# Optimization experiments

Measured on AMD Instinct MI355X. Metric: run time of the kernel, lower is better.

Reference implementation:

```python
import jax, jax.numpy as jnp
import numpy as np

DIM = 768
HEADS = 12
HEAD_DIM = DIM // HEADS
WS = 14  # window size
MLP = 3072
EPS = 1e-6
SCALE = HEAD_DIM ** -0.5
B, H, W = 4, 64, 64


def setup_inputs() -> dict:
    key = jax.random.key(0)
    ks = jax.random.split(key, 8)
    s = 0.02
    f32 = jnp.float32
    return {
        "hidden_states": jax.random.normal(ks[0], (B, DIM, H, W), f32),
        "ln1_w": jnp.ones((DIM,), f32),
        "ln1_b": jnp.zeros((DIM,), f32),
        "qkv_w": jax.random.normal(ks[1], (DIM, 3 * DIM), f32) * s,
        "qkv_b": jnp.zeros((3 * DIM,), f32),
        "proj_w": jax.random.normal(ks[2], (DIM, DIM), f32) * s,
        "proj_b": jnp.zeros((DIM,), f32),
        "rel_pos_h": jax.random.normal(ks[3], (2 * WS - 1, HEAD_DIM), f32) * s,
        "rel_pos_w": jax.random.normal(ks[4], (2 * WS - 1, HEAD_DIM), f32) * s,
        "ln2_w": jnp.ones((DIM,), f32),
        "ln2_b": jnp.zeros((DIM,), f32),
        "fc1_w": jax.random.normal(ks[5], (DIM, MLP), f32) * s,
        "fc1_b": jnp.zeros((MLP,), f32),
        "fc2_w": jax.random.normal(ks[6], (MLP, DIM), f32) * s,
        "fc2_b": jnp.zeros((DIM,), f32),
    }


def _layer_norm(x, w, b):
    mu = jnp.mean(x, axis=-1, keepdims=True)
    var = jnp.mean(jnp.square(x - mu), axis=-1, keepdims=True)
    return (x - mu) * jax.lax.rsqrt(var + EPS) * w + b


def _get_rel_pos(size, rel_pos):
    # q_size == k_size == WS, rel_pos already has 2*WS-1 rows -> pure gather
    coords = jnp.arange(size)[:, None] - jnp.arange(size)[None, :] + (size - 1)
    return rel_pos[coords]  # (size, size, head_dim)


def _attention(x, qkv_w, qkv_b, proj_w, proj_b, rel_pos_h, rel_pos_w):
    nb, h, w, c = x.shape  # windows batch, WS, WS, DIM
    n = h * w
    qkv = x.reshape(nb, n, c) @ qkv_w + qkv_b  # (nb, n, 3*DIM)
    qkv = qkv.reshape(nb, n, 3, HEADS, HEAD_DIM).transpose(2, 0, 3, 1, 4)
    qkv = qkv.reshape(3, nb * HEADS, n, HEAD_DIM)
    q, k, v = qkv[0], qkv[1], qkv[2]
    attn = jnp.einsum('bqc,bkc->bqk', q * SCALE, k)  # (nb*HEADS, n, n)
    # decomposed relative position bias
    Rh = _get_rel_pos(h, rel_pos_h)  # (h, h, hd)
    Rw = _get_rel_pos(w, rel_pos_w)  # (w, w, hd)
    rq = q.reshape(-1, h, w, HEAD_DIM)
    rel_h = jnp.einsum('bhwc,hkc->bhwk', rq, Rh)
    rel_w = jnp.einsum('bhwc,wkc->bhwk', rq, Rw)
    attn = (attn.reshape(-1, h, w, h, w)
            + rel_h[:, :, :, :, None]
            + rel_w[:, :, :, None, :]).reshape(-1, n, n)
    attn = jax.nn.softmax(attn, axis=-1)
    out = attn @ v  # (nb*HEADS, n, hd)
    out = out.reshape(nb, HEADS, h, w, HEAD_DIM).transpose(0, 2, 3, 1, 4)
    out = out.reshape(nb, h, w, c)
    return out @ proj_w + proj_b


def reference(hidden_states, ln1_w, ln1_b, qkv_w, qkv_b, proj_w, proj_b,
              rel_pos_h, rel_pos_w, ln2_w, ln2_b, fc1_w, fc1_b, fc2_w, fc2_b):
    x = hidden_states.transpose(0, 2, 3, 1)  # NCHW -> NHWC
    b, h, w, c = x.shape
    shortcut = x
    x = _layer_norm(x, ln1_w, ln1_b)
    # window partition with padding
    ph = (WS - h % WS) % WS
    pw = (WS - w % WS) % WS
    x = jnp.pad(x, ((0, 0), (0, ph), (0, pw), (0, 0)))
    hp, wp = h + ph, w + pw
    x = x.reshape(b, hp // WS, WS, wp // WS, WS, c).transpose(0, 1, 3, 2, 4, 5)
    windows = x.reshape(-1, WS, WS, c)
    windows = _attention(windows, qkv_w, qkv_b, proj_w, proj_b, rel_pos_h, rel_pos_w)
    # window unpartition + crop
    x = windows.reshape(b, hp // WS, wp // WS, WS, WS, c).transpose(0, 1, 3, 2, 4, 5)
    x = x.reshape(b, hp, wp, c)[:, :h, :w, :]
    x = shortcut + x
    y = _layer_norm(x, ln2_w, ln2_b)
    y = jax.nn.gelu(y @ fc1_w + fc1_b, approximate=False) @ fc2_w + fc2_b
    x = x + y
    return x.transpose(0, 3, 1, 2)  # back to NCHW
```

## Files before the change

kernel.cpp:

```cpp
#include <hip/hip_runtime.h>
#include <cstdint>
#include <cstddef>

#define NIMG   4
#define GRIDSZ 64
#define CH     768
#define NHEAD  12
#define WSZ    14
#define NWINS  100
#define NTOK   196
#define MWIN   19600
#define MREAL  16384
#define MLPC   3072
#define QKSCALE 0.125f

#define KSTR 72
#define VSTR 216
#define PSTR 40

typedef unsigned short u16;
typedef __attribute__((ext_vector_type(8))) short bf16x8;
typedef __attribute__((ext_vector_type(4))) float f32x4;

__device__ __forceinline__ float b2f(u16 u) {
  uint32_t x = (uint32_t)u << 16; float f; __builtin_memcpy(&f, &x, 4); return f;
}
__device__ __forceinline__ u16 f2b(float f) {
  uint32_t x; __builtin_memcpy(&x, &f, 4);
  x += 0x7fffu + ((x >> 16) & 1u);
  return (u16)(x >> 16);
}

__device__ __forceinline__ float fast_gelu(float x) {
  float z  = x * 0.70710678118654752440f;
  float az = fabsf(z);
  float t  = 1.0f / (1.0f + 0.3275911f * az);
  float poly = ((((1.061405429f * t - 1.453152027f) * t + 1.421413741f) * t
                 - 0.284496736f) * t + 0.254829592f) * t;
  float e  = __expf(-az * az);
  float erfv = copysignf(1.0f - poly * e, z);
  return 0.5f * x * (1.0f + erfv);
}

__device__ __forceinline__ void gl_lds16(const u16* g, u16* l) {
  __builtin_amdgcn_global_load_lds(
      (const __attribute__((address_space(1))) unsigned int*)g,
      (__attribute__((address_space(3))) unsigned int*)l, 16, 0, 0);
}

__global__ __launch_bounds__(256) void k_nchw2nhwc(const float* __restrict__ in,
                                                   float* __restrict__ out) {
  __shared__ float tile[32][33];
  int b  = blockIdx.z;
  int g0 = blockIdx.x * 32;
  int c0 = blockIdx.y * 32;
  int tx = threadIdx.x, ty = threadIdx.y;
  const float* ip = in + (size_t)b * CH * 4096;
  float* op = out + (size_t)b * 4096 * CH;
#pragma unroll
  for (int k = 0; k < 32; k += 8)
    tile[ty + k][tx] = ip[(size_t)(c0 + ty + k) * 4096 + g0 + tx];
  __syncthreads();
#pragma unroll
  for (int k = 0; k < 32; k += 8)
    op[(size_t)(g0 + ty + k) * CH + c0 + tx] = tile[tx][ty + k];
}

__global__ __launch_bounds__(256) void k_nhwc2nchw(const float* __restrict__ in,
                                                   float* __restrict__ out) {
  __shared__ float tile[32][33];
  int b  = blockIdx.z;
  int g0 = blockIdx.x * 32;
  int c0 = blockIdx.y * 32;
  int tx = threadIdx.x, ty = threadIdx.y;
  const float* ip = in + (size_t)b * 4096 * CH;
  float* op = out + (size_t)b * CH * 4096;
#pragma unroll
  for (int k = 0; k < 32; k += 8)
    tile[ty + k][tx] = ip[(size_t)(g0 + ty + k) * CH + c0 + tx];
  __syncthreads();
#pragma unroll
  for (int k = 0; k < 32; k += 8)
    op[(size_t)(c0 + ty + k) * 4096 + g0 + tx] = tile[tx][ty + k];
}

__global__ __launch_bounds__(256) void k_wt(const float* __restrict__ in,
                                            u16* __restrict__ out,
                                            int K, int N) {
  __shared__ float t[32][33];
  int n0 = blockIdx.x * 32, k0 = blockIdx.y * 32;
  int tx = threadIdx.x, ty = threadIdx.y;
#pragma unroll
  for (int k = 0; k < 32; k += 8)
    t[ty + k][tx] = in[(size_t)(k0 + ty + k) * N + n0 + tx];
  __syncthreads();
#pragma unroll
  for (int k = 0; k < 32; k += 8)
    out[(size_t)(n0 + ty + k) * K + k0 + tx] = f2b(t[tx][ty + k]);
}

__device__ __forceinline__ float block_sum(float s, float* red) {
  __syncthreads();
#pragma unroll
  for (int off = 32; off > 0; off >>= 1) s += __shfl_down(s, off, 64);
  int wid = threadIdx.x >> 6, lane = threadIdx.x & 63;
  if (lane == 0) red[wid] = s;
  __syncthreads();
  return red[0] + red[1] + red[2] + red[3];
}

__global__ __launch_bounds__(256) void k_ln(const float* __restrict__ x,
                                            const float* __restrict__ wt,
                                            const float* __restrict__ bs,
                                            u16* __restrict__ y,
                                            int window_mode) {
  __shared__ float red[4];
  int row = blockIdx.x, tid = threadIdx.x;
  const float* xp = x + (size_t)row * CH;
  float v0 = xp[tid], v1 = xp[tid + 256], v2 = xp[tid + 512];
  float mu = block_sum(v0 + v1 + v2, red) * (1.0f / 768.0f);
  float d0 = v0 - mu, d1 = v1 - mu, d2 = v2 - mu;
  float var = block_sum(d0 * d0 + d1 * d1 + d2 * d2, red) * (1.0f / 768.0f);
  float rs = rsqrtf(var + 1e-6f);
  int orow = row;
  if (window_mode) {
    int b = row >> 12, hw = row & 4095;
    int h = hw >> 6, wc = hw & 63;
    orow = (b * 25 + (h / WSZ) * 5 + (wc / WSZ)) * NTOK + (h % WSZ) * WSZ + (wc % WSZ);
  }
  u16* yp = y + (size_t)orow * CH;
  yp[tid]       = f2b(d0 * rs * wt[tid]       + bs[tid]);
  yp[tid + 256] = f2b(d1 * rs * wt[tid + 256] + bs[tid + 256]);
  yp[tid + 512] = f2b(d2 * rs * wt[tid + 512] + bs[tid + 512]);
}

__global__ __launch_bounds__(256, 2) void k_gemm_mfma(const u16* __restrict__ A,
                                                      const u16* __restrict__ BT,
                                                      const float* __restrict__ bias,
                                                      void* __restrict__ Cv,
                                                      u16* __restrict__ Vt,
                                                      int M, int N, int K,
                                                      int act, int mode, int row0) {
  __shared__ u16 As[3][256 * 32];
  __shared__ u16 Bs[3][128 * 32];
  int tid  = threadIdx.x;
  int lane = tid & 63, wave = tid >> 6;

  int gx   = gridDim.x;
  int nwg  = gx * gridDim.y;
  int orig = blockIdx.y * gx + blockIdx.x;
  int q = nwg >> 3, r = nwg & 7;
  int xcd = orig & 7, idx = orig >> 3;
  int wgid = (xcd < r ? xcd * (q + 1) : r * (q + 1) + (xcd - r) * q) + idx;
  int bn = wgid % gx, bm = wgid / gx;

  int wm = (wave & 1) * 128, wn = (wave >> 1) * 64;
  int l15 = lane & 15, quad = lane >> 4;
  int xq = (quad ^ ((l15 >> 1) & 3)) * 8;

  f32x4 acc[8][4];
#pragma unroll
  for (int i = 0; i < 8; i++)
#pragma unroll
    for (int j = 0; j < 4; j++) acc[i][j] = (f32x4){0.f, 0.f, 0.f, 0.f};

  const u16* Atile = A + (size_t)bm * 256 * K;
  const u16* Btile = BT + (size_t)bn * 128 * K;

  const int nk = K >> 5;

#define STAGE_SLAB(slot, slab)                                               \
  do {                                                                       \
    int kk_ = (slab) << 5;                                                   \
    _Pragma("unroll")                                                        \
    for (int i = 0; i < 4; ++i) {                                            \
      int c_ = i * 256 + wave * 64 + lane;                                   \
      int row_ = c_ >> 2, gs_ = (c_ & 3) ^ ((c_ >> 3) & 3);                  \
      gl_lds16(Atile + (size_t)row_ * K + kk_ + gs_ * 8,                     \
               &As[(slot)][(i * 256 + wave * 64) * 8]);                      \
    }                                                                        \
    _Pragma("unroll")                                                        \
    for (int i = 0; i < 2; ++i) {                                            \
      int c_ = i * 256 + wave * 64 + lane;                                   \
      int row_ = c_ >> 2, gs_ = (c_ & 3) ^ ((c_ >> 3) & 3);                  \
      gl_lds16(Btile + (size_t)row_ * K + kk_ + gs_ * 8,                     \
               &Bs[(slot)][(i * 256 + wave * 64) * 8]);                      \
    }                                                                        \
  } while (0)

#define COMPUTE_SLAB(slot)                                                   \
  do {                                                                       \
    bf16x8 af[8], bfv[4];                                                    \
    _Pragma("unroll")                                                        \
    for (int mi = 0; mi < 8; mi++)                                           \
      af[mi] = *(const bf16x8*)&As[(slot)][(size_t)(wm + mi * 16 + l15) * 32 \
                                           + xq];                            \
    _Pragma("unroll")                                                        \
    for (int ni = 0; ni < 4; ni++)                                           \
      bfv[ni] = *(const bf16x8*)&Bs[(slot)][(size_t)(wn + ni * 16 + l15) * 32\
                                            + xq];                           \
    _Pragma("unroll")                                                        \
    for (int mi = 0; mi < 8; mi++)                                           \
      _Pragma("unroll")                                                      \
      for (int ni = 0; ni < 4; ni++)                                         \
        acc[mi][ni] = __builtin_amdgcn_mfma_f32_16x16x32_bf16(               \
            bfv[ni], af[mi], acc[mi][ni], 0, 0, 0);                          \
  } while (0)

  STAGE_SLAB(0, 0);
  STAGE_SLAB(1, 1);

  int t = 0;
  for (; t < nk - 1; ++t) {
    asm volatile("s_waitcnt vmcnt(6)" ::: "memory");
    __builtin_amdgcn_s_barrier();
    __builtin_amdgcn_sched_barrier(0);
    if (t + 2 < nk) STAGE_SLAB((t + 2) % 3, t + 2);
    COMPUTE_SLAB(t % 3);
  }
  asm volatile("s_waitcnt vmcnt(0)" ::: "memory");
  __builtin_amdgcn_s_barrier();
  __builtin_amdgcn_sched_barrier(0);
  COMPUTE_SLAB(t % 3);

#undef STAGE_SLAB
#undef COMPUTE_SLAB

#pragma unroll
  for (int mi = 0; mi < 8; mi++) {
    int row = bm * 256 + wm + mi * 16 + l15;
    if (row >= M) continue;
    size_t gbase = 0;
    bool valid = true;
    int wloc = 0, tok = 0;
    if (mode == 2) {
      int rowa = row + row0;
      int widx = rowa / NTOK, tt = rowa % NTOK;
      int b = widx / 25, wq = widx % 25;
      int h = (wq / 5) * WSZ + tt / WSZ;
      int w = (wq % 5) * WSZ + tt % WSZ;
      valid = (h < GRIDSZ) && (w < GRIDSZ);
      gbase = valid ? ((size_t)((b * GRIDSZ + h) * GRIDSZ + w)) * CH : 0;
    }
    if (mode == 3) { wloc = row / NTOK; tok = row - wloc * NTOK; }
#pragma unroll
    for (int ni = 0; ni < 4; ni++) {
      int colb = bn * 128 + wn + ni * 16 + quad * 4;
      float4 b4 = *(const float4*)&bias[colb];
      float v[4] = {acc[mi][ni][0] + b4.x, acc[mi][ni][1] + b4.y,
                    acc[mi][ni][2] + b4.z, acc[mi][ni][3] + b4.w};
      if (act == 1) {
#pragma unroll
        for (int r2 = 0; r2 < 4; r2++) v[r2] = fast_gelu(v[r2]);
      }
      if (mode == 0) {
        ushort4 st = make_ushort4(f2b(v[0]), f2b(v[1]), f2b(v[2]), f2b(v[3]));
        *(ushort4*)((u16*)Cv + (size_t)row * N + colb) = st;
      } else if (mode == 1) {
        float4* p = (float4*)((float*)Cv + (size_t)row * N + colb);
        float4 o = *p;
        o.x += v[0]; o.y += v[1]; o.z += v[2]; o.w += v[3];
        *p = o;
      } else if (mode == 2) {
        if (valid) {
          float4* p = (float4*)((float*)Cv + gbase + colb);
          float4 o = *p;
          o.x += v[0]; o.y += v[1]; o.z += v[2]; o.w += v[3];
          *p = o;
        }
      } else {
        if (colb < 1536) {
          ushort4 st = make_ushort4(f2b(v[0]), f2b(v[1]), f2b(v[2]), f2b(v[3]));
          *(ushort4*)((u16*)Cv + (size_t)row * N + colb) = st;
        } else {
          int vv = colb - 1536, hd = vv >> 6, d = vv & 63;
          u16* vp = Vt + ((size_t)(wloc * NHEAD + hd) * 64 + d) * VSTR + tok;
#pragma unroll
          for (int r2 = 0; r2 < 4; r2++) vp[(size_t)r2 * VSTR] = f2b(v[r2]);
        }
      }
    }
  }
}

__global__ __launch_bounds__(256) void k_relbias(const u16* __restrict__ qkv,
                                                 const float* __restrict__ rel_h,
                                                 const float* __restrict__ rel_w,
                                                 u16* __restrict__ rhg,
                                                 u16* __restrict__ rwg,
                                                 int nrows) {
  int idx = blockIdx.x * 256 + threadIdx.x;
  if (idx >= nrows * NHEAD) return;
  int head = idx % NHEAD, row = idx / NHEAD;
  int wloc = row / NTOK, tok = row - wloc * NTOK;
  const u16* qp = qkv + (size_t)row * (3 * CH) + head * 64;
  float q[64];
#pragma unroll
  for (int d = 0; d < 64; d += 4) {
    ushort4 u4 = *(const ushort4*)(qp + d);
    q[d] = b2f(u4.x); q[d + 1] = b2f(u4.y); q[d + 2] = b2f(u4.z); q[d + 3] = b2f(u4.w);
  }
  int hq = tok / WSZ, wq = tok % WSZ;
  size_t obase = ((size_t)(wloc * NHEAD + head) * NTOK + tok) * 16;
  for (int kk = 0; kk < WSZ; kk++) {
    const float* rh = rel_h + (size_t)(hq - kk + WSZ - 1) * 64;
    const float* rw = rel_w + (size_t)(wq - kk + WSZ - 1) * 64;
    float sh = 0.0f, sw = 0.0f;
#pragma unroll
    for (int d = 0; d < 64; d++) { sh += q[d] * rh[d]; sw += q[d] * rw[d]; }
    rhg[obase + kk] = f2b(sh);
    rwg[obase + kk] = f2b(sw);
  }
}

__global__ __launch_bounds__(256) void k_attn_mfma(const u16* __restrict__ qkv,
                                                   const u16* __restrict__ Vt,
                                                   const u16* __restrict__ rhg,
                                                   const u16* __restrict__ rwg,
                                                   u16* __restrict__ out,
                                                   int win0) {
  __shared__ u16 Ks[NTOK * KSTR];
  __shared__ u16 Vs[64 * VSTR];
  __shared__ u16 Ps[4][16 * PSTR];
  int head = blockIdx.x, wloc = blockIdx.y;
  int tid = threadIdx.x, lane = tid & 63, wave = tid >> 6;
  int l15 = lane & 15, quad = lane >> 4;
  const u16* qbase = qkv + (size_t)wloc * NTOK * (3 * CH) + head * 64;

  for (int c = tid; c < NTOK * 8; c += 256) {
    int tok = c >> 3, part = c & 7;
    uint4 v = *(const uint4*)(qbase + (size_t)tok * (3 * CH) + CH + part * 8);
    *(uint4*)&Ks[tok * KSTR + part * 8] = v;
  }
  const u16* vb = Vt + (size_t)(wloc * NHEAD + head) * 64 * VSTR;
#pragma unroll
  for (int it = 0; it < 7; ++it) {
    int c = it * 256 + tid;
    if (c < 64 * VSTR / 8) gl_lds16(vb + (size_t)c * 8, Vs + ((size_t)it * 256 + wave * 64) * 8);
  }
  __syncthreads();

  const u16* rhp = rhg + ((size_t)(wloc * NHEAD + head) * NTOK) * 16;
  const u16* rwp = rwg + ((size_t)(wloc * NHEAD + head) * NTOK) * 16;
  int winabs = win0 + wloc;

  for (int t16 = wave; t16 < 13; t16 += 4) {
    int qtok = t16 * 16 + l15; if (qtok > NTOK - 1) qtok = NTOK - 1;
    bf16x8 aq0 = *(const bf16x8*)(qbase + (size_t)qtok * (3 * CH) + quad * 8);
    bf16x8 aq1 = *(const bf16x8*)(qbase + (size_t)qtok * (3 * CH) + 32 + quad * 8);

    f32x4 s[13];
#pragma unroll
    for (int ct = 0; ct < 13; ct++) s[ct] = (f32x4){0.f, 0.f, 0.f, 0.f};
#pragma unroll
    for (int ct = 0; ct < 13; ct++) {
      int ktok = ct * 16 + l15; if (ktok > NTOK - 1) ktok = NTOK - 1;
      bf16x8 bk0 = *(const bf16x8*)&Ks[ktok * KSTR + quad * 8];
      bf16x8 bk1 = *(const bf16x8*)&Ks[ktok * KSTR + 32 + quad * 8];
      s[ct] = __builtin_amdgcn_mfma_f32_16x16x32_bf16(aq0, bk0, s[ct], 0, 0, 0);
      s[ct] = __builtin_amdgcn_mfma_f32_16x16x32_bf16(aq1, bk1, s[ct], 0, 0, 0);
    }

    f32x4 o[4];
#pragma unroll
    for (int ni = 0; ni < 4; ni++) o[ni] = (f32x4){0.f, 0.f, 0.f, 0.f};
    float lsum[4] = {0.f, 0.f, 0.f, 0.f};
    int row0t = t16 * 16 + quad * 4;

#pragma unroll
    for (int cc = 0; cc < 7; ++cc) {
#pragma unroll
      for (int half = 0; half < 2; ++half) {
        int ct = cc * 2 + half;
        if (ct < 13) {
          int col = ct * 16 + l15;
          int jh = col / WSZ, jw = col - jh * WSZ;
          bool colok = col < NTOK;
#pragma unroll
          for (int r = 0; r < 4; r++) {
            int rowt = row0t + r; int rowc = rowt > NTOK - 1 ? NTOK - 1 : rowt;
            float bias = b2f(rhp[rowc * 16 + jh]) + b2f(rwp[rowc * 16 + jw]);
            float sv = s[ct][r] * QKSCALE + bias;
            float p = colok ? __expf(sv) : 0.f;
            lsum[r] += p;
            Ps[wave][(quad * 4 + r) * PSTR + half * 16 + l15] = f2b(p);
          }
        } else {
#pragma unroll
          for (int r = 0; r < 4; r++)
            Ps[wave][(quad * 4 + r) * PSTR + half * 16 + l15] = 0;
        }
      }
      bf16x8 pa = *(const bf16x8*)&Ps[wave][l15 * PSTR + quad * 8];
#pragma unroll
      for (int ni = 0; ni < 4; ni++) {
        bf16x8 bv = *(const bf16x8*)&Vs[(ni * 16 + l15) * VSTR + cc * 32 + quad * 8];
        o[ni] = __builtin_amdgcn_mfma_f32_16x16x32_bf16(pa, bv, o[ni], 0, 0, 0);
      }
    }

#pragma unroll
    for (int r = 0; r < 4; r++) {
#pragma unroll
      for (int m = 1; m < 16; m <<= 1) lsum[r] += __shfl_xor(lsum[r], m, 64);
    }

#pragma unroll
    for (int r = 0; r < 4; r++) {
      int rowt = row0t + r;
      if (rowt < NTOK) {
        float inv = 1.0f / lsum[r];
        u16* op = out + ((size_t)winabs * NTOK + rowt) * CH + head * 64;
#pragma unroll
        for (int ni = 0; ni < 4; ni++) op[ni * 16 + l15] = f2b(o[ni][r] * inv);
      }
    }
  }
}

extern "C" void kernel_launch(void* const* d_in, const int* in_sizes, int n_in,
                              void* d_out, int out_size, void* d_ws, size_t ws_size,
                              hipStream_t stream) {
  const float* hidden = (const float*)d_in[0];
  const float* ln1_w  = (const float*)d_in[1];
  const float* ln1_b  = (const float*)d_in[2];
  const float* qkv_w  = (const float*)d_in[3];
  const float* qkv_b  = (const float*)d_in[4];
  const float* proj_w = (const float*)d_in[5];
  const float* proj_b = (const float*)d_in[6];
  const float* rel_h  = (const float*)d_in[7];
  const float* rel_w  = (const float*)d_in[8];
  const float* ln2_w  = (const float*)d_in[9];
  const float* ln2_b  = (const float*)d_in[10];
  const float* fc1_w  = (const float*)d_in[11];
  const float* fc1_b  = (const float*)d_in[12];
  const float* fc2_w  = (const float*)d_in[13];
  const float* fc2_b  = (const float*)d_in[14];
  float* out = (float*)d_out;

  char* ws = (char*)d_ws;
  float* x_nhwc = (float*)ws;
  u16*   R1     = (u16*)(ws + 50331648);
  u16*   qkvT   = (u16*)(ws + 80437248);
  u16*   projT  = qkvT + (size_t)2304 * 768;
  u16*   fc1T   = projT + (size_t)768 * 768;
  u16*   fc2T   = fc1T + (size_t)3072 * 768;
  u16*   R2     = fc2T + (size_t)768 * 3072;
  size_t used   = (size_t)80437248 + 14155776;
  size_t r2e    = ws_size > used ? (ws_size - used) >> 1 : 0;

  const size_t PW_QKV = (size_t)NTOK * 3 * CH;
  const size_t PW_VT  = (size_t)NHEAD * 64 * VSTR;
  const size_t PW_RB  = (size_t)NHEAD * NTOK * 16;
  const size_t perwin = PW_QKV + PW_VT + 2 * PW_RB;
  size_t wc_s = r2e / perwin;
  int Wc = wc_s >= NWINS ? NWINS : (int)wc_s;
  if (Wc < 1) Wc = 1;
  size_t rc_s = (r2e / MLPC / 256) * 256;
  int Rc = rc_s >= MREAL ? MREAL : (int)rc_s;
  if (Rc < 256) Rc = 256;

  u16* Vt  = R2 + (size_t)Wc * PW_QKV;
  u16* rhg = Vt + (size_t)Wc * PW_VT;
  u16* rwg = rhg + (size_t)Wc * PW_RB;

  k_wt<<<dim3(72, 24), dim3(32, 8), 0, stream>>>(qkv_w, qkvT, CH, 3 * CH);
  k_wt<<<dim3(24, 24), dim3(32, 8), 0, stream>>>(proj_w, projT, CH, CH);
  k_wt<<<dim3(96, 24), dim3(32, 8), 0, stream>>>(fc1_w, fc1T, CH, MLPC);
  k_wt<<<dim3(24, 96), dim3(32, 8), 0, stream>>>(fc2_w, fc2T, MLPC, CH);

  hipMemsetAsync(R1, 0, (size_t)MWIN * CH * sizeof(u16), stream);

  k_nchw2nhwc<<<dim3(128, 24, NIMG), dim3(32, 8), 0, stream>>>(hidden, x_nhwc);
  k_ln<<<MREAL, 256, 0, stream>>>(x_nhwc, ln1_w, ln1_b, R1, 1);
  for (int w0 = 0; w0 < NWINS; w0 += Wc) {
    int wc = NWINS - w0 < Wc ? NWINS - w0 : Wc;
    int Mc = wc * NTOK;
    k_gemm_mfma<<<dim3(18, (Mc + 255) / 256), 256, 0, stream>>>(
        R1 + (size_t)w0 * NTOK * CH, qkvT, qkv_b, R2, Vt,
        Mc, 3 * CH, CH, 0, 3, 0);
    k_relbias<<<(Mc * NHEAD + 255) / 256, 256, 0, stream>>>(
        R2, rel_h, rel_w, rhg, rwg, Mc);
    k_attn_mfma<<<dim3(NHEAD, wc), 256, 0, stream>>>(
        R2, Vt, rhg, rwg, R1, w0);
  }
  k_gemm_mfma<<<dim3(6, (MWIN + 255) / 256), 256, 0, stream>>>(
      R1, projT, proj_b, x_nhwc, nullptr, MWIN, CH, CH, 0, 2, 0);
  k_ln<<<MREAL, 256, 0, stream>>>(x_nhwc, ln2_w, ln2_b, R1, 0);
  for (int r0 = 0; r0 < MREAL; r0 += Rc) {
    int rc = MREAL - r0 < Rc ? MREAL - r0 : Rc;
    k_gemm_mfma<<<dim3(24, (rc + 255) / 256), 256, 0, stream>>>(
        R1 + (size_t)r0 * CH, fc1T, fc1_b, R2, nullptr, rc, MLPC, CH, 1, 0, 0);
    k_gemm_mfma<<<dim3(6, (rc + 255) / 256), 256, 0, stream>>>(
        R2, fc2T, fc2_b, x_nhwc + (size_t)r0 * CH, nullptr, rc, CH, MLPC, 0, 1, 0);
  }
  k_nhwc2nchw<<<dim3(128, 24, NIMG), dim3(32, 8), 0, stream>>>(x_nhwc, out);
}
```

Baseline: 765.9 us.

## Template GEMM on M-tile size and use 128-row tiles for narrow-N GEMMs

Turns the MFMA GEMM into a template over the M-tile height and occupancy hint. The N=768 GEMMs (proj and fc2) now use 128-row tiles with three blocks per CU, giving more workgroups to fill the GPU. The k-loop is also unrolled by three so the LDS slot indices are compile-time constants, and the per-slab global addresses are precomputed pointers that are bumped each step. The trade-off is lower reuse per tile in the smaller variant, and the unrolled loop assumes the K-slab count fits the three-slot pattern.

```diff
diff --git a/kernel.cpp b/kernel.cpp
--- a/kernel.cpp
+++ b/kernel.cpp
@@ -134,14 +134,18 @@
   yp[tid + 512] = f2b(d2 * rs * wt[tid + 512] + bs[tid + 512]);
 }
 
-__global__ __launch_bounds__(256, 2) void k_gemm_mfma(const u16* __restrict__ A,
+template <int BMT, int MINB>
+__global__ __launch_bounds__(256, MINB) void k_gemm_t(const u16* __restrict__ A,
                                                       const u16* __restrict__ BT,
                                                       const float* __restrict__ bias,
                                                       void* __restrict__ Cv,
                                                       u16* __restrict__ Vt,
                                                       int M, int N, int K,
                                                       int act, int mode, int row0) {
-  __shared__ u16 As[3][256 * 32];
+  constexpr int MI = BMT / 32;
+  constexpr int LA = BMT / 64;
+  constexpr int L  = LA + 2;
+  __shared__ u16 As[3][BMT * 32];
   __shared__ u16 Bs[3][128 * 32];
   int tid  = threadIdx.x;
   int lane = tid & 63, wave = tid >> 6;
@@ -154,81 +158,95 @@
   int wgid = (xcd < r ? xcd * (q + 1) : r * (q + 1) + (xcd - r) * q) + idx;
   int bn = wgid % gx, bm = wgid / gx;
 
-  int wm = (wave & 1) * 128, wn = (wave >> 1) * 64;
+  int wm = (wave & 1) * (BMT / 2), wn = (wave >> 1) * 64;
   int l15 = lane & 15, quad = lane >> 4;
   int xq = (quad ^ ((l15 >> 1) & 3)) * 8;
 
-  f32x4 acc[8][4];
-#pragma unroll
-  for (int i = 0; i < 8; i++)
+  f32x4 acc[MI][4];
+#pragma unroll
+  for (int i = 0; i < MI; i++)
 #pragma unroll
     for (int j = 0; j < 4; j++) acc[i][j] = (f32x4){0.f, 0.f, 0.f, 0.f};
 
-  const u16* Atile = A + (size_t)bm * 256 * K;
+  const u16* Atile = A + (size_t)bm * BMT * K;
   const u16* Btile = BT + (size_t)bn * 128 * K;
 
+  const u16* ga[LA];
+  const u16* gb[2];
+#pragma unroll
+  for (int i = 0; i < LA; ++i) {
+    int c_ = i * 256 + wave * 64 + lane;
+    int row_ = c_ >> 2, gs_ = (c_ & 3) ^ ((c_ >> 3) & 3);
+    ga[i] = Atile + (size_t)row_ * K + gs_ * 8;
+  }
+#pragma unroll
+  for (int i = 0; i < 2; ++i) {
+    int c_ = i * 256 + wave * 64 + lane;
+    int row_ = c_ >> 2, gs_ = (c_ & 3) ^ ((c_ >> 3) & 3);
+    gb[i] = Btile + (size_t)row_ * K + gs_ * 8;
+  }
+
   const int nk = K >> 5;
 
-#define STAGE_SLAB(slot, slab)                                               \
+#define STAGE(slot)                                                          \
   do {                                                                       \
-    int kk_ = (slab) << 5;                                                   \
     _Pragma("unroll")                                                        \
-    for (int i = 0; i < 4; ++i) {                                            \
-      int c_ = i * 256 + wave * 64 + lane;                                   \
-      int row_ = c_ >> 2, gs_ = (c_ & 3) ^ ((c_ >> 3) & 3);                  \
-      gl_lds16(Atile + (size_t)row_ * K + kk_ + gs_ * 8,                     \
-               &As[(slot)][(i * 256 + wave * 64) * 8]);                      \
+    for (int i = 0; i < LA; ++i) {                                           \
+      gl_lds16(ga[i], &As[(slot)][(i * 256 + wave * 64) * 8]);               \
+      ga[i] += 32;                                                           \
     }                                                                        \
     _Pragma("unroll")                                                        \
     for (int i = 0; i < 2; ++i) {                                            \
-      int c_ = i * 256 + wave * 64 + lane;                                   \
-      int row_ = c_ >> 2, gs_ = (c_ & 3) ^ ((c_ >> 3) & 3);                  \
-      gl_lds16(Btile + (size_t)row_ * K + kk_ + gs_ * 8,                     \
-               &Bs[(slot)][(i * 256 + wave * 64) * 8]);                      \
+      gl_lds16(gb[i], &Bs[(slot)][(i * 256 + wave * 64) * 8]);               \
+      gb[i] += 32;                                                           \
     }                                                                        \
   } while (0)
 
-#define COMPUTE_SLAB(slot)                                                   \
+#define COMPUTE(slot)                                                        \
   do {                                                                       \
-    bf16x8 af[8], bfv[4];                                                    \
+    bf16x8 af[MI], bfv[4];                                                   \
     _Pragma("unroll")                                                        \
-    for (int mi = 0; mi < 8; mi++)                                           \
-      af[mi] = *(const bf16x8*)&As[(slot)][(size_t)(wm + mi * 16 + l15) * 32 \
-                                           + xq];                            \
+    for (int mi = 0; mi < MI; mi++)                                          \
+      af[mi] = *(const bf16x8*)&As[(slot)][(wm + mi * 16 + l15) * 32 + xq];  \
     _Pragma("unroll")                                                        \
     for (int ni = 0; ni < 4; ni++)                                           \
-      bfv[ni] = *(const bf16x8*)&Bs[(slot)][(size_t)(wn + ni * 16 + l15) * 32\
-                                            + xq];                           \
+      bfv[ni] = *(const bf16x8*)&Bs[(slot)][(wn + ni * 16 + l15) * 32 + xq]; \
     _Pragma("unroll")                                                        \
-    for (int mi = 0; mi < 8; mi++)                                           \
+    for (int mi = 0; mi < MI; mi++)                                          \
       _Pragma("unroll")                                                      \
       for (int ni = 0; ni < 4; ni++)                                         \
         acc[mi][ni] = __builtin_amdgcn_mfma_f32_16x16x32_bf16(               \
             bfv[ni], af[mi], acc[mi][ni], 0, 0, 0);                          \
   } while (0)
 
-  STAGE_SLAB(0, 0);
-  STAGE_SLAB(1, 1);
-
-  int t = 0;
-  for (; t < nk - 1; ++t) {
-    asm volatile("s_waitcnt vmcnt(6)" ::: "memory");
-    __builtin_amdgcn_s_barrier();
-    __builtin_amdgcn_sched_barrier(0);
-    if (t + 2 < nk) STAGE_SLAB((t + 2) % 3, t + 2);
-    COMPUTE_SLAB(t % 3);
-  }
+#define WAITL                                                                \
+  do {                                                                       \
+    if constexpr (L == 6) asm volatile("s_waitcnt vmcnt(6)" ::: "memory");   \
+    else                  asm volatile("s_waitcnt vmcnt(4)" ::: "memory");   \
+    __builtin_amdgcn_s_barrier();                                            \
+  } while (0)
+
+  STAGE(0);
+  STAGE(1);
+
+  for (int g = 0; g < nk - 3; g += 3) {
+    WAITL; STAGE(2); COMPUTE(0);
+    WAITL; STAGE(0); COMPUTE(1);
+    WAITL; STAGE(1); COMPUTE(2);
+  }
+  WAITL; STAGE(2); COMPUTE(0);
+  WAITL;           COMPUTE(1);
   asm volatile("s_waitcnt vmcnt(0)" ::: "memory");
   __builtin_amdgcn_s_barrier();
-  __builtin_amdgcn_sched_barrier(0);
-  COMPUTE_SLAB(t % 3);
-
-#undef STAGE_SLAB
-#undef COMPUTE_SLAB
-
-#pragma unroll
-  for (int mi = 0; mi < 8; mi++) {
-    int row = bm * 256 + wm + mi * 16 + l15;
+  COMPUTE(2);
+
+#undef STAGE
+#undef COMPUTE
+#undef WAITL
+
+#pragma unroll
+  for (int mi = 0; mi < MI; mi++) {
+    int row = bm * BMT + wm + mi * 16 + l15;
     if (row >= M) continue;
     size_t gbase = 0;
     bool valid = true;
@@ -476,7 +494,7 @@
   for (int w0 = 0; w0 < NWINS; w0 += Wc) {
     int wc = NWINS - w0 < Wc ? NWINS - w0 : Wc;
     int Mc = wc * NTOK;
-    k_gemm_mfma<<<dim3(18, (Mc + 255) / 256), 256, 0, stream>>>(
+    k_gemm_t<256, 2><<<dim3(18, (Mc + 255) / 256), 256, 0, stream>>>(
         R1 + (size_t)w0 * NTOK * CH, qkvT, qkv_b, R2, Vt,
         Mc, 3 * CH, CH, 0, 3, 0);
     k_relbias<<<(Mc * NHEAD + 255) / 256, 256, 0, stream>>>(
@@ -484,14 +502,14 @@
     k_attn_mfma<<<dim3(NHEAD, wc), 256, 0, stream>>>(
         R2, Vt, rhg, rwg, R1, w0);
   }
-  k_gemm_mfma<<<dim3(6, (MWIN + 255) / 256), 256, 0, stream>>>(
+  k_gemm_t<128, 3><<<dim3(6, (MWIN + 127) / 128), 256, 0, stream>>>(
       R1, projT, proj_b, x_nhwc, nullptr, MWIN, CH, CH, 0, 2, 0);
   k_ln<<<MREAL, 256, 0, stream>>>(x_nhwc, ln2_w, ln2_b, R1, 0);
   for (int r0 = 0; r0 < MREAL; r0 += Rc) {
     int rc = MREAL - r0 < Rc ? MREAL - r0 : Rc;
-    k_gemm_mfma<<<dim3(24, (rc + 255) / 256), 256, 0, stream>>>(
+    k_gemm_t<256, 2><<<dim3(24, (rc + 255) / 256), 256, 0, stream>>>(
         R1 + (size_t)r0 * CH, fc1T, fc1_b, R2, nullptr, rc, MLPC, CH, 1, 0, 0);
-    k_gemm_mfma<<<dim3(6, (rc + 255) / 256), 256, 0, stream>>>(
+    k_gemm_t<128, 3><<<dim3(6, (rc + 127) / 128), 256, 0, stream>>>(
         R2, fc2T, fc2_b, x_nhwc + (size_t)r0 * CH, nullptr, rc, CH, MLPC, 0, 1, 0);
   }
   k_nhwc2nchw<<<dim3(128, 24, NIMG), dim3(32, 8), 0, stream>>>(x_nhwc, out);
```

New measurement: 761.9 us. About the same (-0.5%).
